# Optimization experiments

Hardware: AMD Instinct MI355X
Metric: run time of the kernel (lower is better)

The kernel has to match this reference:

```python
import jax, jax.numpy as jnp
import numpy as np

NUM_SEGMENTS = 2048  # matches fill_max of superpixels_results


def setup_inputs() -> dict:
    key = jax.random.key(0)
    k1, k2 = jax.random.split(key)
    B, C, H, W = 2, 64, 1024, 1024
    superpixels_results = jax.random.randint(k1, (B, H, W), 0, NUM_SEGMENTS, dtype=jnp.int32)
    feats = jax.random.normal(k2, (B, C, H, W), dtype=jnp.float32)
    return {"superpixels_results": superpixels_results, "feats": feats}


def reference(superpixels_results, feats):
    # Faithful to the original torch code: `return` sits inside the batch loop,
    # so ONLY batch 0 is processed, and c counts unique ids of batch 0 only.
    C = feats.shape[1]
    sp = superpixels_results[0].reshape(-1)            # [P] int segment ids
    x = feats[0].reshape(C, -1).T                      # [P, C]

    seg_sum = jax.ops.segment_sum(x, sp, num_segments=NUM_SEGMENTS)        # [S, C]
    seg_sumsq = jax.ops.segment_sum(x * x, sp, num_segments=NUM_SEGMENTS)  # [S, C]
    counts = jax.ops.segment_sum(jnp.ones_like(sp, dtype=x.dtype), sp,
                                 num_segments=NUM_SEGMENTS)                # [S]

    n = jnp.maximum(counts, 1.0)[:, None]              # avoid div-by-zero
    # sum over pixels of (x - mean)^2, per segment and channel:
    var_sum = seg_sumsq - seg_sum * seg_sum / n        # [S, C]
    # original does var_loss_t.mean() over [C, n] elements:
    per_seg = var_sum.sum(axis=1) / (C * jnp.maximum(counts, 1.0))  # [S]

    valid = counts >= 2.0                              # segments with <2 px skipped
    var_loss = jnp.where(valid, per_seg, 0.0).sum()
    c = (counts > 0.0).sum().astype(x.dtype)           # unique ids in batch 0
    return var_loss / c
```

## Files before the change

kernel.cpp:

```cpp
#include <hip/hip_runtime.h>

#define S_SEG 2048
#define C_ALL 64
#define P_PIX (1024 * 1024)
#define CH_PER 4
#define N_GROUPS 16
#define N_CHUNKS 64
#define BLOCK 512
#define PIX_PER_BLOCK (P_PIX / N_CHUNKS)

#define OFF_SQ   131072
#define OFF_CNT  133120
#define N_ZERO   135168

__global__ void zero_kernel(float* __restrict__ p, int n) {
    int i = blockIdx.x * blockDim.x + threadIdx.x;
    if (i < n) p[i] = 0.0f;
}

__global__ __launch_bounds__(256) void count_kernel(const int* __restrict__ sp,
                                                    int* __restrict__ cnt_g) {
    __shared__ int cnt_h[S_SEG];
    const int tid = threadIdx.x;
    for (int i = tid; i < S_SEG; i += 256) cnt_h[i] = 0;
    __syncthreads();
    const int base = blockIdx.x * (P_PIX / 256);
    const int4* sp4 = (const int4*)(sp + base);
    const int iters = (P_PIX / 256) / (256 * 4);
    for (int it = 0; it < iters; ++it) {
        const int4 s4 = sp4[it * 256 + tid];
        atomicAdd(&cnt_h[s4.x], 1);
        atomicAdd(&cnt_h[s4.y], 1);
        atomicAdd(&cnt_h[s4.z], 1);
        atomicAdd(&cnt_h[s4.w], 1);
    }
    __syncthreads();
    for (int i = tid; i < S_SEG; i += 256) {
        const int v = cnt_h[i];
        if (v != 0) atomicAdd(&cnt_g[i], v);
    }
}

__global__ __launch_bounds__(BLOCK) void accum_kernel(
        const int* __restrict__ sp, const float* __restrict__ feats,
        float* __restrict__ sum_g, float* __restrict__ sq_g) {
    __shared__ float hist[CH_PER * S_SEG];
    __shared__ float sq_h[S_SEG];
    const int tid = threadIdx.x;
    const int chunk = blockIdx.x;
    const int grp = blockIdx.y;
    const int c0 = grp * CH_PER;

    for (int i = tid; i < CH_PER * S_SEG; i += BLOCK) hist[i] = 0.0f;
    for (int i = tid; i < S_SEG; i += BLOCK) sq_h[i] = 0.0f;
    __syncthreads();

    const int base = chunk * PIX_PER_BLOCK;
    const int4* sp4 = (const int4*)(sp + base);
    const int iters = PIX_PER_BLOCK / (BLOCK * 4);

    for (int it = 0; it < iters; ++it) {
        const int idx = it * BLOCK + tid;
        const int4 s4 = sp4[idx];
        float sq0 = 0.f, sq1 = 0.f, sq2 = 0.f, sq3 = 0.f;
#pragma unroll
        for (int c = 0; c < CH_PER; ++c) {
            const float4 v =
                ((const float4*)(feats + (size_t)(c0 + c) * P_PIX + base))[idx];
            unsafeAtomicAdd(&hist[c * S_SEG + s4.x], v.x); sq0 = fmaf(v.x, v.x, sq0);
            unsafeAtomicAdd(&hist[c * S_SEG + s4.y], v.y); sq1 = fmaf(v.y, v.y, sq1);
            unsafeAtomicAdd(&hist[c * S_SEG + s4.z], v.z); sq2 = fmaf(v.z, v.z, sq2);
            unsafeAtomicAdd(&hist[c * S_SEG + s4.w], v.w); sq3 = fmaf(v.w, v.w, sq3);
        }
        unsafeAtomicAdd(&sq_h[s4.x], sq0);
        unsafeAtomicAdd(&sq_h[s4.y], sq1);
        unsafeAtomicAdd(&sq_h[s4.z], sq2);
        unsafeAtomicAdd(&sq_h[s4.w], sq3);
    }
    __syncthreads();

    for (int i = tid; i < CH_PER * S_SEG; i += BLOCK) {
        const int c = i >> 11, s = i & (S_SEG - 1);
        const float v = hist[i];
        if (v != 0.0f) unsafeAtomicAdd(&sum_g[(size_t)(c0 + c) * S_SEG + s], v);
    }
    for (int i = tid; i < S_SEG; i += BLOCK) {
        const float v = sq_h[i];
        if (v != 0.0f) unsafeAtomicAdd(&sq_g[i], v);
    }
}

__global__ __launch_bounds__(1024) void finalize_kernel(
        const float* __restrict__ sum_g, const float* __restrict__ sq_g,
        const int* __restrict__ cnt_g, float* __restrict__ out) {
    __shared__ float red_l[16], red_c[16];
    const int tid = threadIdx.x;
    float loss = 0.0f, cc = 0.0f;
#pragma unroll
    for (int k = 0; k < 2; ++k) {
        const int s = tid + k * 1024;
        const float cnt = (float)cnt_g[s];
        const float n = fmaxf(cnt, 1.0f);
        float acc = 0.0f;
#pragma unroll 8
        for (int c = 0; c < C_ALL; ++c) {
            const float v = sum_g[c * S_SEG + s];
            acc = fmaf(v, v, acc);
        }
        const float var = sq_g[s] - acc / n;
        loss += (cnt >= 2.0f) ? var / (64.0f * n) : 0.0f;
        cc += (cnt > 0.0f) ? 1.0f : 0.0f;
    }
    for (int off = 32; off; off >>= 1) {
        loss += __shfl_down(loss, off);
        cc += __shfl_down(cc, off);
    }
    const int wave = tid >> 6;
    if ((tid & 63) == 0) { red_l[wave] = loss; red_c[wave] = cc; }
    __syncthreads();
    if (tid < 16) {
        loss = red_l[tid]; cc = red_c[tid];
        for (int off = 8; off; off >>= 1) {
            loss += __shfl_down(loss, off);
            cc += __shfl_down(cc, off);
        }
        if (tid == 0) out[0] = loss / cc;
    }
}

extern "C" void kernel_launch(void* const* d_in, const int* in_sizes, int n_in,
                              void* d_out, int out_size, void* d_ws, size_t ws_size,
                              hipStream_t stream) {
    const int* sp = (const int*)d_in[0];
    const float* feats = (const float*)d_in[1];
    float* ws = (float*)d_ws;
    float* sum_g = ws;
    float* sq_g = ws + OFF_SQ;
    int* cnt_g = (int*)(ws + OFF_CNT);

    zero_kernel<<<(N_ZERO + 255) / 256, 256, 0, stream>>>(ws, N_ZERO);

    count_kernel<<<256, 256, 0, stream>>>(sp, cnt_g);

    dim3 grid(N_CHUNKS, N_GROUPS);
    accum_kernel<<<grid, BLOCK, 0, stream>>>(sp, feats, sum_g, sq_g);

    finalize_kernel<<<1, 1024, 0, stream>>>(sum_g, sq_g, cnt_g, (float*)d_out);
}
```

Before: 972.1 us.

## Replace LDS atomic histogramming with counting-sort scatter and per-segment reduction

Adds a path that counts pixels per segment per quarter, prefix-sums offsets, scatters features into segment-sorted pixel-major order in the workspace, then reduces each segment with one block and no feature atomics. This targets contention from the shared-memory float atomics in the previous accumulate kernel. In exchange it writes and rereads a 64 MB sorted copy of the features per quarter and launches more kernels. It falls back to the old path when the workspace is too small.

```diff
diff --git a/kernel.cpp b/kernel.cpp
--- a/kernel.cpp
+++ b/kernel.cpp
@@ -3,20 +3,213 @@
 #define S_SEG 2048
 #define C_ALL 64
 #define P_PIX (1024 * 1024)
+
+
+#define NQ 4
+#define PQ (P_PIX / NQ)
+#define FS_WORDS (PQ * C_ALL)
+
+#define W_SUM  FS_WORDS
+#define W_SQ   (W_SUM + S_SEG * C_ALL)
+#define W_CNTQ (W_SQ + S_SEG)
+#define W_CNTT (W_CNTQ + NQ * S_SEG)
+#define W_OFF  (W_CNTT + S_SEG)
+#define W_CUR  (W_OFF + NQ * S_SEG)
+#define W_END  (W_CUR + NQ * S_SEG)
+#define ZERO2_WORDS (S_SEG * C_ALL + S_SEG + NQ * S_SEG)
+#define NEEDED_BYTES ((size_t)W_END * 4)
+
+#define SC_CHUNK 512
+#define SC_THREADS 512
+#define SC_BLOCKS (PQ / SC_CHUNK)
+
+__global__ void zero_kernel(float* __restrict__ p, int n) {
+    int i = blockIdx.x * blockDim.x + threadIdx.x;
+    if (i < n) p[i] = 0.0f;
+}
+
+__global__ __launch_bounds__(256) void countq_kernel(const int* __restrict__ sp,
+                                                     int* __restrict__ cnt_q) {
+    __shared__ int h[S_SEG];
+    const int tid = threadIdx.x;
+    for (int i = tid; i < S_SEG; i += 256) h[i] = 0;
+    __syncthreads();
+    const int base = blockIdx.x * 4096;
+    const int4* sp4 = (const int4*)(sp + base);
+    for (int it = 0; it < 4; ++it) {
+        const int4 s4 = sp4[it * 256 + tid];
+        atomicAdd(&h[s4.x], 1);
+        atomicAdd(&h[s4.y], 1);
+        atomicAdd(&h[s4.z], 1);
+        atomicAdd(&h[s4.w], 1);
+    }
+    __syncthreads();
+    int* dst = cnt_q + (blockIdx.x >> 6) * S_SEG;
+    for (int i = tid; i < S_SEG; i += 256) {
+        const int v = h[i];
+        if (v != 0) atomicAdd(&dst[i], v);
+    }
+}
+
+__global__ __launch_bounds__(1024) void prefix_kernel(const int* __restrict__ cnt_q,
+                                                      int* __restrict__ cnt_tot,
+                                                      int* __restrict__ off_q,
+                                                      int* __restrict__ cur_q) {
+    __shared__ int a[S_SEG], b[S_SEG];
+    const int tid = threadIdx.x;
+    for (int i = tid; i < S_SEG; i += 1024) {
+        int t = 0;
+        for (int q = 0; q < NQ; ++q) t += cnt_q[q * S_SEG + i];
+        cnt_tot[i] = t;
+    }
+    for (int q = 0; q < NQ; ++q) {
+        for (int i = tid; i < S_SEG; i += 1024) a[i] = cnt_q[q * S_SEG + i];
+        __syncthreads();
+        int* src = a;
+        int* dst = b;
+        for (int d = 1; d < S_SEG; d <<= 1) {
+            for (int i = tid; i < S_SEG; i += 1024)
+                dst[i] = src[i] + (i >= d ? src[i - d] : 0);
+            __syncthreads();
+            int* t = src; src = dst; dst = t;
+        }
+        for (int i = tid; i < S_SEG; i += 1024) {
+            const int e = i ? src[i - 1] : 0;
+            off_q[q * S_SEG + i] = e;
+            cur_q[q * S_SEG + i] = e;
+        }
+        __syncthreads();
+    }
+}
+
+__global__ __launch_bounds__(SC_THREADS) void scatter_kernel(
+        const int* __restrict__ sp, const float* __restrict__ feats,
+        int* __restrict__ cur_q, float* __restrict__ featsS, int q) {
+    __shared__ int lh[S_SEG];
+    __shared__ int lpos[SC_CHUNK];
+    __shared__ float tile[C_ALL][129];
+    const int tid = threadIdx.x;
+    const int pixbase = q * PQ + blockIdx.x * SC_CHUNK;
+
+    for (int i = tid; i < S_SEG; i += SC_THREADS) lh[i] = 0;
+    __syncthreads();
+    const int seg = sp[pixbase + tid];
+    atomicAdd(&lh[seg], 1);
+    __syncthreads();
+    int* cur = cur_q + q * S_SEG;
+    for (int i = tid; i < S_SEG; i += SC_THREADS) {
+        const int c = lh[i];
+        if (c != 0) lh[i] = atomicAdd(&cur[i], c);
+    }
+    __syncthreads();
+    lpos[tid] = atomicAdd(&lh[seg], 1);
+    __syncthreads();
+
+    const int wave = tid >> 6, lane = tid & 63;
+    for (int t0 = 0; t0 < SC_CHUNK; t0 += 128) {
+        for (int k = tid; k < 2048; k += SC_THREADS) {
+            const int c = k >> 5;
+            const int x = (k & 31) << 2;
+            const float4 v = *(const float4*)(feats + (size_t)c * P_PIX + pixbase + t0 + x);
+            tile[c][x + 0] = v.x; tile[c][x + 1] = v.y;
+            tile[c][x + 2] = v.z; tile[c][x + 3] = v.w;
+        }
+        __syncthreads();
+        for (int t = wave; t < 128; t += 8) {
+            const int p = lpos[t0 + t];
+            featsS[(size_t)p * 64 + lane] = tile[lane][t];
+        }
+        __syncthreads();
+    }
+}
+
+__global__ __launch_bounds__(256) void accumq_kernel(
+        const float* __restrict__ featsS, const int* __restrict__ cnt_q,
+        const int* __restrict__ off_q, float* __restrict__ sum_sc,
+        float* __restrict__ sq_s, int q) {
+    const int seg = blockIdx.x;
+    const int n = cnt_q[q * S_SEG + seg];
+    if (n == 0) return;
+    const int start = off_q[q * S_SEG + seg];
+    const int wave = threadIdx.x >> 6, lane = threadIdx.x & 63;
+    const float* base = featsS + (size_t)start * 64 + lane;
+    float a0 = 0.f, a1 = 0.f, s0 = 0.f, s1 = 0.f;
+    int i = wave;
+    for (; i + 4 < n; i += 8) {
+        const float v0 = base[(size_t)i * 64];
+        const float v1 = base[(size_t)(i + 4) * 64];
+        a0 += v0; s0 = fmaf(v0, v0, s0);
+        a1 += v1; s1 = fmaf(v1, v1, s1);
+    }
+    for (; i < n; i += 4) {
+        const float v = base[(size_t)i * 64];
+        a0 += v; s0 = fmaf(v, v, s0);
+    }
+    __shared__ float pr[4][64];
+    __shared__ float psq[4];
+    pr[wave][lane] = a0 + a1;
+    float sq = s0 + s1;
+    for (int off = 32; off; off >>= 1) sq += __shfl_down(sq, off);
+    if (lane == 0) psq[wave] = sq;
+    __syncthreads();
+    if (wave == 0) {
+        const float tot = pr[0][lane] + pr[1][lane] + pr[2][lane] + pr[3][lane];
+        sum_sc[(size_t)seg * 64 + lane] += tot;
+        if (lane == 0) sq_s[seg] += psq[0] + psq[1] + psq[2] + psq[3];
+    }
+}
+
+__global__ __launch_bounds__(1024) void finalizeq_kernel(
+        const float* __restrict__ sum_sc, const float* __restrict__ sq_s,
+        const int* __restrict__ cnt_tot, float* __restrict__ out) {
+    __shared__ float red_l[16], red_c[16];
+    const int tid = threadIdx.x;
+    float loss = 0.0f, cc = 0.0f;
+#pragma unroll
+    for (int k = 0; k < 2; ++k) {
+        const int s = tid + k * 1024;
+        const float cnt = (float)cnt_tot[s];
+        const float n = fmaxf(cnt, 1.0f);
+        const float4* r = (const float4*)(sum_sc + (size_t)s * 64);
+        float acc = 0.0f;
+#pragma unroll
+        for (int c4 = 0; c4 < 16; ++c4) {
+            const float4 v = r[c4];
+            acc = fmaf(v.x, v.x, acc);
+            acc = fmaf(v.y, v.y, acc);
+            acc = fmaf(v.z, v.z, acc);
+            acc = fmaf(v.w, v.w, acc);
+        }
+        const float var = sq_s[s] - acc / n;
+        loss += (cnt >= 2.0f) ? var / (64.0f * n) : 0.0f;
+        cc += (cnt > 0.0f) ? 1.0f : 0.0f;
+    }
+    for (int off = 32; off; off >>= 1) {
+        loss += __shfl_down(loss, off);
+        cc += __shfl_down(cc, off);
+    }
+    const int wave = tid >> 6;
+    if ((tid & 63) == 0) { red_l[wave] = loss; red_c[wave] = cc; }
+    __syncthreads();
+    if (tid < 16) {
+        loss = red_l[tid]; cc = red_c[tid];
+        for (int off = 8; off; off >>= 1) {
+            loss += __shfl_down(loss, off);
+            cc += __shfl_down(cc, off);
+        }
+        if (tid == 0) out[0] = loss / cc;
+    }
+}
+
+
 #define CH_PER 4
 #define N_GROUPS 16
 #define N_CHUNKS 64
 #define BLOCK 512
 #define PIX_PER_BLOCK (P_PIX / N_CHUNKS)
-
 #define OFF_SQ   131072
 #define OFF_CNT  133120
 #define N_ZERO   135168
-
-__global__ void zero_kernel(float* __restrict__ p, int n) {
-    int i = blockIdx.x * blockDim.x + threadIdx.x;
-    if (i < n) p[i] = 0.0f;
-}
 
 __global__ __launch_bounds__(256) void count_kernel(const int* __restrict__ sp,
                                                     int* __restrict__ cnt_g) {
@@ -128,22 +321,40 @@
     }
 }
 
+
 extern "C" void kernel_launch(void* const* d_in, const int* in_sizes, int n_in,
                               void* d_out, int out_size, void* d_ws, size_t ws_size,
                               hipStream_t stream) {
     const int* sp = (const int*)d_in[0];
     const float* feats = (const float*)d_in[1];
     float* ws = (float*)d_ws;
-    float* sum_g = ws;
-    float* sq_g = ws + OFF_SQ;
-    int* cnt_g = (int*)(ws + OFF_CNT);
-
-    zero_kernel<<<(N_ZERO + 255) / 256, 256, 0, stream>>>(ws, N_ZERO);
-
-    count_kernel<<<256, 256, 0, stream>>>(sp, cnt_g);
-
-    dim3 grid(N_CHUNKS, N_GROUPS);
-    accum_kernel<<<grid, BLOCK, 0, stream>>>(sp, feats, sum_g, sq_g);
-
-    finalize_kernel<<<1, 1024, 0, stream>>>(sum_g, sq_g, cnt_g, (float*)d_out);
-}
+
+    if (ws_size >= NEEDED_BYTES) {
+        float* featsS = ws;
+        float* sum_sc = ws + W_SUM;
+        float* sq_s   = ws + W_SQ;
+        int* cnt_q    = (int*)(ws + W_CNTQ);
+        int* cnt_tot  = (int*)(ws + W_CNTT);
+        int* off_q    = (int*)(ws + W_OFF);
+        int* cur_q    = (int*)(ws + W_CUR);
+
+        zero_kernel<<<(ZERO2_WORDS + 255) / 256, 256, 0, stream>>>(ws + W_SUM, ZERO2_WORDS);
+        countq_kernel<<<256, 256, 0, stream>>>(sp, cnt_q);
+        prefix_kernel<<<1, 1024, 0, stream>>>(cnt_q, cnt_tot, off_q, cur_q);
+        for (int q = 0; q < NQ; ++q) {
+            scatter_kernel<<<SC_BLOCKS, SC_THREADS, 0, stream>>>(sp, feats, cur_q, featsS, q);
+            accumq_kernel<<<S_SEG, 256, 0, stream>>>(featsS, cnt_q, off_q, sum_sc, sq_s, q);
+        }
+        finalizeq_kernel<<<1, 1024, 0, stream>>>(sum_sc, sq_s, cnt_tot, (float*)d_out);
+    } else {
+        float* sum_g = ws;
+        float* sq_g = ws + OFF_SQ;
+        int* cnt_g = (int*)(ws + OFF_CNT);
+
+        zero_kernel<<<(N_ZERO + 255) / 256, 256, 0, stream>>>(ws, N_ZERO);
+        count_kernel<<<256, 256, 0, stream>>>(sp, cnt_g);
+        dim3 grid(N_CHUNKS, N_GROUPS);
+        accum_kernel<<<grid, BLOCK, 0, stream>>>(sp, feats, sum_g, sq_g);
+        finalize_kernel<<<1, 1024, 0, stream>>>(sum_g, sq_g, cnt_g, (float*)d_out);
+    }
+}
```

After: 823.2 us. 1.18x faster.
